# Performance work log

Hardware: AMD Instinct MI355X
Metric: run time of the kernel (lower is better)

The kernel has to match this reference:

```python
import jax, jax.numpy as jnp
import numpy as np

D_MODEL = 1024
H = 16
D_K = D_MODEL // H
B, S = 1, 4096


def setup_inputs() -> dict:
    key = jax.random.key(0)
    ks = jax.random.split(key, 12)
    std = 1.0 / np.sqrt(D_MODEL)
    inp = {
        "q": jax.random.normal(ks[0], (B, S, D_MODEL), dtype=jnp.float32),
        "k": jax.random.normal(ks[1], (B, S, D_MODEL), dtype=jnp.float32),
        "v": jax.random.normal(ks[2], (B, S, D_MODEL), dtype=jnp.float32),
        "mask": jax.random.randint(ks[3], (B, 1, S, S), 0, 2).astype(bool),
        # nn.Linear params (torch convention: y = x @ W.T + b), weights [out, in]
        "wq": jax.random.uniform(ks[4], (D_MODEL, D_MODEL), jnp.float32, -std, std),
        "bq": jax.random.uniform(ks[5], (D_MODEL,), jnp.float32, -std, std),
        "wk": jax.random.uniform(ks[6], (D_MODEL, D_MODEL), jnp.float32, -std, std),
        "bk": jax.random.uniform(ks[7], (D_MODEL,), jnp.float32, -std, std),
        "wv": jax.random.uniform(ks[8], (D_MODEL, D_MODEL), jnp.float32, -std, std),
        "bv": jax.random.uniform(ks[9], (D_MODEL,), jnp.float32, -std, std),
        "wo": jax.random.uniform(ks[10], (D_MODEL, D_MODEL), jnp.float32, -std, std),
        "bo": jax.random.uniform(ks[11], (D_MODEL,), jnp.float32, -std, std),
    }
    return inp


def _split_heads(x):
    # [b, s, (h d)] -> [b, h, s, d]
    b, s, _ = x.shape
    return x.reshape(b, s, H, D_K).transpose(0, 2, 1, 3)


def reference(q, k, v, mask, wq, bq, wk, bk, wv, bv, wo, bo):
    b, s, d = q.shape
    qh = _split_heads(q @ wq.T + bq)
    kh = _split_heads(k @ wk.T + bk)
    vh = _split_heads(v @ wv.T + bv)
    # NOTE: original scales by sqrt(d_model), not sqrt(d_k) — keep faithful.
    score = jnp.einsum("bhqd,bhkd->bhqk", qh, kh) / jnp.sqrt(jnp.float32(d))
    score = jnp.where(mask, jnp.float32(-1e9), score)
    attn = jax.nn.softmax(score, axis=-1)  # dropout is identity in eval mode
    wv_out = jnp.einsum("bhqk,bhkd->bhqd", attn, vh)
    concat = wv_out.transpose(0, 2, 1, 3).reshape(b, s, d)
    return concat @ wo.T + bo
```

## Files before the change

kernel.cpp:

```cpp
#include <hip/hip_runtime.h>
#include <hip/hip_bf16.h>
#include <math.h>

typedef __attribute__((ext_vector_type(4))) float f32x4;
typedef __attribute__((ext_vector_type(8))) short s16x8;
typedef __attribute__((ext_vector_type(4))) short s16x4;

#define S_LEN 4096
#define DMODEL 1024
#define NHEADS 16
#define DHEAD 64

__device__ __forceinline__ unsigned short f2bf(float f) {
  union { float f; unsigned int u; } x; x.f = f;
  return (unsigned short)((x.u + 0x7FFFu + ((x.u >> 16) & 1u)) >> 16);
}

__device__ __forceinline__ float fexp2(float x) {
#if __has_builtin(__builtin_amdgcn_exp2f)
  return __builtin_amdgcn_exp2f(x);
#else
  float r; asm("v_exp_f32 %0, %1" : "=v"(r) : "v"(x)); return r;
#endif
}

__device__ __forceinline__ void gload_lds16(const void* g, void* l) {
  __builtin_amdgcn_global_load_lds(
      (const __attribute__((address_space(1))) unsigned int*)g,
      (__attribute__((address_space(3))) unsigned int*)l, 16, 0, 0);
}

__global__ __launch_bounds__(256) void mask_pack(const int* __restrict__ mask,
                                                 unsigned long long* __restrict__ bits) {
  const int qr = blockIdx.x;
  const int wv = threadIdx.x >> 6, l = threadIdx.x & 63;
  const int* row = mask + (size_t)qr * S_LEN;
#pragma unroll
  for (int w0 = 0; w0 < 64; w0 += 4) {
    const int w = w0 + wv;
    unsigned long long b = __ballot(row[w * 64 + l] != 0);
    if (l == 0) bits[(size_t)qr * 64 + w] = b;
  }
}

__global__ __launch_bounds__(256) void mask_xpose(const unsigned long long* __restrict__ bits,
                                                  unsigned long long* __restrict__ lmask) {
  const int wv = blockIdx.x * 4 + (threadIdx.x >> 6);
  const int l = threadIdx.x & 63, lr = l & 15, lg4 = (l >> 4) * 4;
  const int qg = wv >> 6, t = wv & 63;
  const unsigned long long rw = bits[(size_t)(qg * 16 + lr) * 64 + t];
  unsigned long long mine = 0;
#pragma unroll
  for (int w = 0; w < 16; ++w) {
    const int sh = (w >> 2) * 16 + (w & 3) + lg4;
    unsigned long long b = __ballot(((rw >> sh) & 1ull) != 0);
    if (l == w) mine = b;
  }
  if (l < 16) lmask[((size_t)qg * 64 + t) * 16 + l] = mine;
}

__global__ __launch_bounds__(256) void cast_bf16(
    const float* __restrict__ s0, const float* __restrict__ s1, const float* __restrict__ s2,
    const float* __restrict__ s3, const float* __restrict__ s4, const float* __restrict__ s5,
    const float* __restrict__ s6, unsigned short* __restrict__ dst) {
  const int z = blockIdx.y;
  const float* src = (z == 0) ? s0 : (z == 1) ? s1 : (z == 2) ? s2 :
                     (z == 3) ? s3 : (z == 4) ? s4 : (z == 5) ? s5 : s6;
  const int n = (z < 3) ? (S_LEN * DMODEL) : (DMODEL * DMODEL);
  unsigned short* d = dst + ((z < 3) ? (size_t)z * S_LEN * DMODEL
                                     : (size_t)3 * S_LEN * DMODEL + (size_t)(z - 3) * DMODEL * DMODEL);
  const int i = (blockIdx.x * 256 + threadIdx.x) * 4;
  if (i < n) {
    f32x4 v = *(const f32x4*)(src + i);
    s16x4 o;
#pragma unroll
    for (int j = 0; j < 4; ++j) o[j] = (short)f2bf(v[j]);
    *(s16x4*)(d + i) = o;
  }
}

template<int A_BF16, int B_BF16, int OUT_MODE>
__device__ __forceinline__ void gemm_body(const void* __restrict__ Ap,
                                          const void* __restrict__ Wp,
                                          const float* __restrict__ bias,
                                          void* __restrict__ outp, float scale) {
  constexpr int K = DMODEL, N = DMODEL, M = S_LEN;
  constexpr int BM = 128, BK = 32, LDT = 40;
  __shared__ unsigned short Alds[BM * LDT];
  __shared__ unsigned short Blds[BM * LDT];
  const int tid = threadIdx.x;
  const int l = tid & 63, wid = tid >> 6;
  const int lr = l & 15, lg = l >> 4;
  const int bm = blockIdx.x * BM;
  const int bn = blockIdx.y * BM;
  const int wm = (wid >> 1) * 64, wn = (wid & 1) * 64;

  f32x4 acc[4][4] = {};

  for (int k0 = 0; k0 < K; k0 += BK) {
    __syncthreads();
    if constexpr (A_BF16) {
      const unsigned short* A = (const unsigned short*)Ap;
      const int col = (tid & 3) * 8, row = tid >> 2;
#pragma unroll
      for (int p = 0; p < 2; ++p) {
        const int r = row + p * 64;
        *(s16x8*)&Alds[r * LDT + col] =
            *(const s16x8*)(A + (size_t)(bm + r) * K + k0 + col);
      }
    } else {
      const float* A = (const float*)Ap;
      const int col = (tid & 7) * 4, row = tid >> 3;
#pragma unroll
      for (int p = 0; p < 4; ++p) {
        const int r = row + p * 32;
        f32x4 vv = *(const f32x4*)(A + (size_t)(bm + r) * K + k0 + col);
        s16x4 o;
#pragma unroll
        for (int j = 0; j < 4; ++j) o[j] = (short)f2bf(vv[j]);
        *(s16x4*)&Alds[r * LDT + col] = o;
      }
    }
    if constexpr (B_BF16) {
      const unsigned short* W = (const unsigned short*)Wp;
      const int col = (tid & 3) * 8, row = tid >> 2;
#pragma unroll
      for (int p = 0; p < 2; ++p) {
        const int r = row + p * 64;
        *(s16x8*)&Blds[r * LDT + col] =
            *(const s16x8*)(W + (size_t)(bn + r) * K + k0 + col);
      }
    } else {
      const float* W = (const float*)Wp;
      const int col = (tid & 7) * 4, row = tid >> 3;
#pragma unroll
      for (int p = 0; p < 4; ++p) {
        const int r = row + p * 32;
        f32x4 vv = *(const f32x4*)(W + (size_t)(bn + r) * K + k0 + col);
        s16x4 o;
#pragma unroll
        for (int j = 0; j < 4; ++j) o[j] = (short)f2bf(vv[j]);
        *(s16x4*)&Blds[r * LDT + col] = o;
      }
    }
    __syncthreads();
    s16x8 af[4], bfr[4];
#pragma unroll
    for (int mi = 0; mi < 4; ++mi)
      af[mi] = *(const s16x8*)&Alds[(wm + mi * 16 + lr) * LDT + lg * 8];
#pragma unroll
    for (int ni = 0; ni < 4; ++ni)
      bfr[ni] = *(const s16x8*)&Blds[(wn + ni * 16 + lr) * LDT + lg * 8];
#pragma unroll
    for (int mi = 0; mi < 4; ++mi)
#pragma unroll
      for (int ni = 0; ni < 4; ++ni)
        acc[mi][ni] = __builtin_amdgcn_mfma_f32_16x16x32_bf16(af[mi], bfr[ni], acc[mi][ni], 0, 0, 0);
  }

#pragma unroll
  for (int ni = 0; ni < 4; ++ni) {
    const int n = bn + wn + ni * 16 + lr;
    const float bv = bias[n];
#pragma unroll
    for (int mi = 0; mi < 4; ++mi) {
#pragma unroll
      for (int j = 0; j < 4; ++j) {
        const int m = bm + wm + mi * 16 + lg * 4 + j;
        const float val = (acc[mi][ni][j] + bv) * scale;
        if constexpr (OUT_MODE == 1) {
          unsigned short* out = (unsigned short*)outp;
          out[((size_t)(n >> 6) * M + m) * DHEAD + (n & 63)] = f2bf(val);
        } else if constexpr (OUT_MODE == 2) {
          unsigned short* out = (unsigned short*)outp;
          out[((size_t)(n >> 6) * DHEAD + (n & 63)) * M + m] = f2bf(val);
        } else {
          float* out = (float*)outp;
          out[(size_t)m * N + n] = val;
        }
      }
    }
  }
}

#define QSCALE 0.04508422f

__global__ __launch_bounds__(256) void proj_qkv_b16(
    const unsigned short* __restrict__ qb, const unsigned short* __restrict__ kb,
    const unsigned short* __restrict__ vb,
    const unsigned short* __restrict__ wqb, const float* __restrict__ bq,
    const unsigned short* __restrict__ wkb, const float* __restrict__ bk,
    const unsigned short* __restrict__ wvb, const float* __restrict__ bv,
    unsigned short* __restrict__ ws) {
  const int z = blockIdx.z;
  if (z == 0)      gemm_body<1, 1, 1>(qb, wqb, bq, ws, QSCALE);
  else if (z == 1) gemm_body<1, 1, 1>(kb, wkb, bk, ws + (size_t)S_LEN * DMODEL, 1.0f);
  else             gemm_body<1, 1, 2>(vb, wvb, bv, ws + (size_t)2 * S_LEN * DMODEL, 1.0f);
}
__global__ __launch_bounds__(256) void proj_qkv_f32(
    const float* __restrict__ q, const float* __restrict__ k, const float* __restrict__ v,
    const float* __restrict__ wq, const float* __restrict__ bq,
    const float* __restrict__ wk, const float* __restrict__ bk,
    const float* __restrict__ wv, const float* __restrict__ bv,
    unsigned short* __restrict__ ws) {
  const int z = blockIdx.z;
  if (z == 0)      gemm_body<0, 0, 1>(q, wq, bq, ws, QSCALE);
  else if (z == 1) gemm_body<0, 0, 1>(k, wk, bk, ws + (size_t)S_LEN * DMODEL, 1.0f);
  else             gemm_body<0, 0, 2>(v, wv, bv, ws + (size_t)2 * S_LEN * DMODEL, 1.0f);
}
__global__ __launch_bounds__(256) void outproj_b16(
    const unsigned short* __restrict__ concat, const unsigned short* __restrict__ wob,
    const float* __restrict__ bo, float* __restrict__ out) {
  gemm_body<1, 1, 0>(concat, wob, bo, out, 1.0f);
}
__global__ __launch_bounds__(256) void outproj_f32(
    const unsigned short* __restrict__ concat, const float* __restrict__ wo,
    const float* __restrict__ bo, float* __restrict__ out) {
  gemm_body<1, 0, 0>(concat, wo, bo, out, 1.0f);
}

template<int NSPLIT>
__global__ __launch_bounds__(512, 4) void attn_fwd(
    const unsigned short* __restrict__ Qh, const unsigned short* __restrict__ Kh,
    const unsigned short* __restrict__ Vt, const unsigned long long* __restrict__ lmask,
    unsigned short* __restrict__ outp,
    float* __restrict__ lpart) {
  __shared__ unsigned short Klds[2][64 * 64];
  __shared__ unsigned short Vlds[2][64 * 64];
  __shared__ unsigned short P_lds[8][32][72];

  const int tid = threadIdx.x;
  const int l = tid & 63, wid = tid >> 6;
  const int lr = l & 15, lg = l >> 4;
  const int per = 32 * NSPLIT;
  const int swz = (blockIdx.x & 7) * per + (blockIdx.x >> 3);
  const int h = swz / (16 * NSPLIT);
  const int split = (NSPLIT == 2) ? ((swz >> 4) & 1) : 0;
  const int qb = swz & 15;
  const int qrow0 = qb * 256 + wid * 32;
  const int kv0 = split * (S_LEN / NSPLIT);
  constexpr int NT = (S_LEN / NSPLIT) / 64;
  const int T0 = kv0 >> 6;

  const unsigned short* Qbase = Qh + ((size_t)h * S_LEN + qrow0) * DHEAD;
  s16x8 qf[2][2];
#pragma unroll
  for (int sub = 0; sub < 2; ++sub)
#pragma unroll
    for (int ds = 0; ds < 2; ++ds)
      qf[sub][ds] = *(const s16x8*)(Qbase + (sub * 16 + lr) * DHEAD + ds * 32 + lg * 8);

  const int wid_u = __builtin_amdgcn_readfirstlane(wid);
  const int qg0 = qb * 16 + wid_u * 2;
  const unsigned long long* mq0 = lmask + (size_t)qg0 * 64 * 16;
  const unsigned long long* mq1 = mq0 + (size_t)64 * 16;

  const int srow = l >> 3;
  const int schunk = (l & 7) ^ srow;
  const unsigned short* Kst = Kh + (size_t)h * S_LEN * DHEAD
                              + (size_t)(kv0 + wid * 8 + srow) * DHEAD + schunk * 8;
  const unsigned short* Vst = Vt + (size_t)h * DHEAD * S_LEN
                              + (size_t)(wid * 8 + srow) * S_LEN + kv0 + schunk * 8;
  const int sdst = (wid * 8) * 64;

  f32x4 o_acc[2][4] = {};
  float lsum[2] = {0.f, 0.f};

  gload_lds16(Kst, &Klds[0][sdst]);
  gload_lds16(Vst, &Vlds[0][sdst]);
  __syncthreads();

  const int xr = lr & 7;

  for (int t = 0; t < NT; ++t) {
    const int buf = t & 1;
    if (t < NT - 1) {
      gload_lds16(Kst + (size_t)(t + 1) * 64 * DHEAD, &Klds[buf ^ 1][sdst]);
      gload_lds16(Vst + (t + 1) * 64, &Vlds[buf ^ 1][sdst]);
    }

    const unsigned short* Kb = &Klds[buf][0];
    f32x4 sc[2][4];
    __builtin_amdgcn_s_setprio(1);
#pragma unroll
    for (int kg = 0; kg < 4; ++kg) {
      const int r = kg * 16 + lr;
      s16x8 k0 = *(const s16x8*)(Kb + r * 64 + ((lg ^ xr) * 8));
      s16x8 k1 = *(const s16x8*)(Kb + r * 64 + (((lg + 4) ^ xr) * 8));
#pragma unroll
      for (int sub = 0; sub < 2; ++sub) {
        f32x4 z = {};
        z = __builtin_amdgcn_mfma_f32_16x16x32_bf16(k0, qf[sub][0], z, 0, 0, 0);
        sc[sub][kg] = __builtin_amdgcn_mfma_f32_16x16x32_bf16(k1, qf[sub][1], z, 0, 0, 0);
      }
    }
    __builtin_amdgcn_s_setprio(0);

    const size_t mo = (size_t)(T0 + t) * 16;
#pragma unroll
    for (int sub = 0; sub < 2; ++sub) {
      const unsigned long long* qp = (sub ? mq1 : mq0) + mo;
#pragma unroll
      for (int kg = 0; kg < 4; ++kg) {
        float p[4];
#pragma unroll
        for (int j = 0; j < 4; ++j) {
          const unsigned long long mw = qp[kg * 4 + j];
          float pv = fexp2(sc[sub][kg][j]);
          asm("v_cndmask_b32 %0, %1, 0, %2" : "=v"(pv) : "v"(pv), "s"(mw));
          p[j] = pv;
          lsum[sub] += pv;
        }
        unsigned int w0, w1;
        asm("v_cvt_pk_bf16_f32 %0, %1, %2" : "=v"(w0) : "v"(p[0]), "v"(p[1]));
        asm("v_cvt_pk_bf16_f32 %0, %1, %2" : "=v"(w1) : "v"(p[2]), "v"(p[3]));
        uint2 pk; pk.x = w0; pk.y = w1;
        *(uint2*)&P_lds[wid][sub * 16 + lr][kg * 16 + lg * 4] = pk;
      }
    }
    asm volatile("s_waitcnt lgkmcnt(0)" ::: "memory");
    __builtin_amdgcn_sched_barrier(0);

    s16x8 pf[2][2];
#pragma unroll
    for (int sub = 0; sub < 2; ++sub)
#pragma unroll
      for (int ks = 0; ks < 2; ++ks)
        pf[sub][ks] = *(const s16x8*)&P_lds[wid][sub * 16 + lr][ks * 32 + lg * 8];

    const unsigned short* Vb = &Vlds[buf][0];
    __builtin_amdgcn_s_setprio(1);
#pragma unroll
    for (int dg = 0; dg < 4; ++dg) {
      const int r = dg * 16 + lr;
      s16x8 v0 = *(const s16x8*)(Vb + r * 64 + ((lg ^ xr) * 8));
      s16x8 v1 = *(const s16x8*)(Vb + r * 64 + (((lg + 4) ^ xr) * 8));
#pragma unroll
      for (int sub = 0; sub < 2; ++sub) {
        o_acc[sub][dg] = __builtin_amdgcn_mfma_f32_16x16x32_bf16(pf[sub][0], v0, o_acc[sub][dg], 0, 0, 0);
        o_acc[sub][dg] = __builtin_amdgcn_mfma_f32_16x16x32_bf16(pf[sub][1], v1, o_acc[sub][dg], 0, 0, 0);
      }
    }
    __builtin_amdgcn_s_setprio(0);

    __syncthreads();
  }

#pragma unroll
  for (int sub = 0; sub < 2; ++sub) {
    lsum[sub] += __shfl_xor(lsum[sub], 16, 64);
    lsum[sub] += __shfl_xor(lsum[sub], 32, 64);
  }

  if constexpr (NSPLIT == 2) {
    unsigned short* op = outp + ((size_t)(split * NHEADS + h) * S_LEN) * DHEAD;
#pragma unroll
    for (int sub = 0; sub < 2; ++sub)
#pragma unroll
      for (int dg = 0; dg < 4; ++dg)
#pragma unroll
        for (int j = 0; j < 4; ++j) {
          const int q = qrow0 + sub * 16 + lg * 4 + j;
          op[(size_t)q * DHEAD + dg * 16 + lr] = f2bf(o_acc[sub][dg][j]);
        }
    if (l < 16) {
      float* lp = lpart + (size_t)(split * NHEADS + h) * S_LEN + qrow0;
      lp[lr] = lsum[0];
      lp[16 + lr] = lsum[1];
    }
  } else {
    float rs[2][4];
#pragma unroll
    for (int sub = 0; sub < 2; ++sub)
#pragma unroll
      for (int j = 0; j < 4; ++j)
        rs[sub][j] = __shfl(lsum[sub], lg * 4 + j, 64);
#pragma unroll
    for (int sub = 0; sub < 2; ++sub)
#pragma unroll
      for (int dg = 0; dg < 4; ++dg)
#pragma unroll
        for (int j = 0; j < 4; ++j) {
          const int q = qrow0 + sub * 16 + lg * 4 + j;
          outp[(size_t)q * DMODEL + h * DHEAD + dg * 16 + lr] =
              f2bf(o_acc[sub][dg][j] / rs[sub][j]);
        }
  }
}

__global__ __launch_bounds__(256) void attn_combine(
    const unsigned short* __restrict__ opart, const float* __restrict__ lpart,
    unsigned short* __restrict__ concat) {
  const int idx = blockIdx.x * 256 + threadIdx.x;
  const int d4 = (idx & 15) * 4;
  const int hq = idx >> 4;
  const int h = hq >> 12, q = hq & 4095;
  const size_t o0 = ((size_t)h * S_LEN + q) * DHEAD + d4;
  const size_t o1 = o0 + (size_t)NHEADS * S_LEN * DHEAD;
  const float linv = 1.0f / (lpart[(size_t)h * S_LEN + q] +
                             lpart[(size_t)(NHEADS + h) * S_LEN + q]);
  s16x4 a = *(const s16x4*)(opart + o0);
  s16x4 b = *(const s16x4*)(opart + o1);
  s16x4 r;
#pragma unroll
  for (int i = 0; i < 4; ++i) {
    union { unsigned int u; float f; } xa, xb;
    xa.u = ((unsigned int)(unsigned short)a[i]) << 16;
    xb.u = ((unsigned int)(unsigned short)b[i]) << 16;
    r[i] = (short)f2bf((xa.f + xb.f) * linv);
  }
  *(s16x4*)(concat + ((size_t)q * DMODEL + h * DHEAD + d4)) = r;
}

extern "C" void kernel_launch(void* const* d_in, const int* in_sizes, int n_in,
                              void* d_out, int out_size, void* d_ws, size_t ws_size,
                              hipStream_t stream) {
  const float* q  = (const float*)d_in[0];
  const float* k  = (const float*)d_in[1];
  const float* v  = (const float*)d_in[2];
  const int* mask = (const int*)d_in[3];
  const float* wq = (const float*)d_in[4];
  const float* bq = (const float*)d_in[5];
  const float* wk = (const float*)d_in[6];
  const float* bk = (const float*)d_in[7];
  const float* wv = (const float*)d_in[8];
  const float* bv = (const float*)d_in[9];
  const float* wo = (const float*)d_in[10];
  const float* bo = (const float*)d_in[11];
  float* out = (float*)d_out;

  const size_t SD = (size_t)S_LEN * DMODEL, DD = (size_t)DMODEL * DMODEL;
  unsigned short* wsq = (unsigned short*)d_ws;
  unsigned short* wsc = wsq + 3 * SD;
  unsigned long long* wsbits = (unsigned long long*)(wsc + SD);
  unsigned long long* wslm = wsbits + (size_t)S_LEN * 64;
  unsigned short* cast0 = (unsigned short*)(wslm + (size_t)256 * 64 * 16);
  const size_t need = (size_t)((char*)(cast0 + 3 * SD + 4 * DD) - (char*)d_ws);
  const bool big = ws_size >= need;

  mask_pack<<<dim3(S_LEN), dim3(256), 0, stream>>>(mask, wsbits);
  mask_xpose<<<dim3(4096), dim3(256), 0, stream>>>(wsbits, wslm);

  if (big) {
    unsigned short* qb  = cast0;
    unsigned short* kb  = qb + SD;
    unsigned short* vb  = kb + SD;
    unsigned short* wqb = vb + SD;
    unsigned short* wkb = wqb + DD;
    unsigned short* wvb = wkb + DD;
    unsigned short* wob = wvb + DD;
    unsigned short* opart = cast0;
    float* lpart = (float*)vb;
    cast_bf16<<<dim3(4096, 7), dim3(256), 0, stream>>>(q, k, v, wq, wk, wv, wo, cast0);
    proj_qkv_b16<<<dim3(32, 8, 3), dim3(256), 0, stream>>>(qb, kb, vb, wqb, bq, wkb, bk, wvb, bv, wsq);
    attn_fwd<2><<<dim3(512), dim3(512), 0, stream>>>(wsq, wsq + SD, wsq + 2 * SD, wslm, opart, lpart);
    attn_combine<<<dim3(4096), dim3(256), 0, stream>>>(opart, lpart, wsc);
    outproj_b16<<<dim3(32, 8), dim3(256), 0, stream>>>(wsc, wob, bo, out);
  } else {
    proj_qkv_f32<<<dim3(32, 8, 3), dim3(256), 0, stream>>>(q, k, v, wq, bq, wk, bk, wv, bv, wsq);
    attn_fwd<1><<<dim3(256), dim3(512), 0, stream>>>(wsq, wsq + SD, wsq + 2 * SD, wslm, wsc, nullptr);
    outproj_f32<<<dim3(32, 8), dim3(256), 0, stream>>>(wsc, wo, bo, out);
  }
}
```

Before: 199.1 us.

## Fuse mask packing into one kernel and use direct-to-LDS loads in bf16 GEMM

Measured after the change: 219.1 us. 10.1% more time.

```diff
diff --git a/kernel.cpp b/kernel.cpp
--- a/kernel.cpp
+++ b/kernel.cpp
@@ -30,33 +30,22 @@
       (__attribute__((address_space(3))) unsigned int*)l, 16, 0, 0);
 }
 
-__global__ __launch_bounds__(256) void mask_pack(const int* __restrict__ mask,
-                                                 unsigned long long* __restrict__ bits) {
-  const int qr = blockIdx.x;
+__global__ __launch_bounds__(256) void mask_lane(const int* __restrict__ mask,
+                                                 unsigned long long* __restrict__ lmask) {
+  const int qg = blockIdx.x;
   const int wv = threadIdx.x >> 6, l = threadIdx.x & 63;
-  const int* row = mask + (size_t)qr * S_LEN;
-#pragma unroll
-  for (int w0 = 0; w0 < 64; w0 += 4) {
-    const int w = w0 + wv;
-    unsigned long long b = __ballot(row[w * 64 + l] != 0);
-    if (l == 0) bits[(size_t)qr * 64 + w] = b;
-  }
-}
-
-__global__ __launch_bounds__(256) void mask_xpose(const unsigned long long* __restrict__ bits,
-                                                  unsigned long long* __restrict__ lmask) {
-  const int wv = blockIdx.x * 4 + (threadIdx.x >> 6);
-  const int l = threadIdx.x & 63, lr = l & 15, lg4 = (l >> 4) * 4;
-  const int qg = wv >> 6, t = wv & 63;
-  const unsigned long long rw = bits[(size_t)(qg * 16 + lr) * 64 + t];
-  unsigned long long mine = 0;
-#pragma unroll
-  for (int w = 0; w < 16; ++w) {
-    const int sh = (w >> 2) * 16 + (w & 3) + lg4;
-    unsigned long long b = __ballot(((rw >> sh) & 1ull) != 0);
-    if (l == w) mine = b;
-  }
-  if (l < 16) lmask[((size_t)qg * 64 + t) * 16 + l] = mine;
+  const int lr = l & 15, lg = l >> 4;
+  const int* base = mask + (size_t)(qg * 16 + lr) * S_LEN;
+  for (int t = wv; t < 64; t += 4) {
+#pragma unroll
+    for (int kg = 0; kg < 4; ++kg) {
+#pragma unroll
+      for (int j = 0; j < 4; ++j) {
+        unsigned long long b = __ballot(base[t * 64 + kg * 16 + lg * 4 + j] != 0);
+        if (l == 0) lmask[((size_t)qg * 64 + t) * 16 + kg * 4 + j] = b;
+      }
+    }
+  }
 }
 
 __global__ __launch_bounds__(256) void cast_bf16(
@@ -79,78 +68,46 @@
   }
 }
 
-template<int A_BF16, int B_BF16, int OUT_MODE>
-__device__ __forceinline__ void gemm_body(const void* __restrict__ Ap,
-                                          const void* __restrict__ Wp,
-                                          const float* __restrict__ bias,
-                                          void* __restrict__ outp, float scale) {
+template<int OUT_MODE>
+__device__ __forceinline__ void gemm_b16_body(const unsigned short* __restrict__ A,
+                                              const unsigned short* __restrict__ W,
+                                              const float* __restrict__ bias,
+                                              void* __restrict__ outp, float scale) {
   constexpr int K = DMODEL, N = DMODEL, M = S_LEN;
-  constexpr int BM = 128, BK = 32, LDT = 40;
-  __shared__ unsigned short Alds[BM * LDT];
-  __shared__ unsigned short Blds[BM * LDT];
+  constexpr int BM = 128, BK = 32;
+  __shared__ unsigned short Alds[BM * BK];
+  __shared__ unsigned short Blds[BM * BK];
   const int tid = threadIdx.x;
   const int l = tid & 63, wid = tid >> 6;
   const int lr = l & 15, lg = l >> 4;
-  const int bm = blockIdx.x * BM;
-  const int bn = blockIdx.y * BM;
+  const int bm = blockIdx.x * BM, bn = blockIdx.y * BM;
   const int wm = (wid >> 1) * 64, wn = (wid & 1) * 64;
 
+  const int srow = tid >> 2;
+  const int schunk = (tid & 3) ^ (srow & 3);
+  const unsigned short* As = A + (size_t)(bm + srow) * K + schunk * 8;
+  const unsigned short* Ws = W + (size_t)(bn + srow) * K + schunk * 8;
+  unsigned short* Ald = &Alds[srow * BK + (tid & 3) * 8];
+  unsigned short* Bld = &Blds[srow * BK + (tid & 3) * 8];
+
   f32x4 acc[4][4] = {};
+  const int xc = (lg ^ (lr & 3)) * 8;
 
   for (int k0 = 0; k0 < K; k0 += BK) {
     __syncthreads();
-    if constexpr (A_BF16) {
-      const unsigned short* A = (const unsigned short*)Ap;
-      const int col = (tid & 3) * 8, row = tid >> 2;
-#pragma unroll
-      for (int p = 0; p < 2; ++p) {
-        const int r = row + p * 64;
-        *(s16x8*)&Alds[r * LDT + col] =
-            *(const s16x8*)(A + (size_t)(bm + r) * K + k0 + col);
-      }
-    } else {
-      const float* A = (const float*)Ap;
-      const int col = (tid & 7) * 4, row = tid >> 3;
-#pragma unroll
-      for (int p = 0; p < 4; ++p) {
-        const int r = row + p * 32;
-        f32x4 vv = *(const f32x4*)(A + (size_t)(bm + r) * K + k0 + col);
-        s16x4 o;
-#pragma unroll
-        for (int j = 0; j < 4; ++j) o[j] = (short)f2bf(vv[j]);
-        *(s16x4*)&Alds[r * LDT + col] = o;
-      }
-    }
-    if constexpr (B_BF16) {
-      const unsigned short* W = (const unsigned short*)Wp;
-      const int col = (tid & 3) * 8, row = tid >> 2;
-#pragma unroll
-      for (int p = 0; p < 2; ++p) {
-        const int r = row + p * 64;
-        *(s16x8*)&Blds[r * LDT + col] =
-            *(const s16x8*)(W + (size_t)(bn + r) * K + k0 + col);
-      }
-    } else {
-      const float* W = (const float*)Wp;
-      const int col = (tid & 7) * 4, row = tid >> 3;
-#pragma unroll
-      for (int p = 0; p < 4; ++p) {
-        const int r = row + p * 32;
-        f32x4 vv = *(const f32x4*)(W + (size_t)(bn + r) * K + k0 + col);
-        s16x4 o;
-#pragma unroll
-        for (int j = 0; j < 4; ++j) o[j] = (short)f2bf(vv[j]);
-        *(s16x4*)&Blds[r * LDT + col] = o;
-      }
-    }
+    gload_lds16(As + k0, Ald);
+    gload_lds16(As + (size_t)64 * K + k0, Ald + 64 * BK);
+    gload_lds16(Ws + k0, Bld);
+    gload_lds16(Ws + (size_t)64 * K + k0, Bld + 64 * BK);
     __syncthreads();
+
     s16x8 af[4], bfr[4];
 #pragma unroll
     for (int mi = 0; mi < 4; ++mi)
-      af[mi] = *(const s16x8*)&Alds[(wm + mi * 16 + lr) * LDT + lg * 8];
+      af[mi] = *(const s16x8*)&Alds[(wm + mi * 16 + lr) * BK + xc];
 #pragma unroll
     for (int ni = 0; ni < 4; ++ni)
-      bfr[ni] = *(const s16x8*)&Blds[(wn + ni * 16 + lr) * LDT + lg * 8];
+      bfr[ni] = *(const s16x8*)&Blds[(wn + ni * 16 + lr) * BK + xc];
 #pragma unroll
     for (int mi = 0; mi < 4; ++mi)
 #pragma unroll
@@ -183,6 +140,101 @@
   }
 }
 
+template<int A_BF16, int OUT_MODE>
+__device__ __forceinline__ void gemm_f32_body(const void* __restrict__ Ap,
+                                              const float* __restrict__ W,
+                                              const float* __restrict__ bias,
+                                              void* __restrict__ outp, float scale) {
+  constexpr int K = DMODEL, N = DMODEL, M = S_LEN;
+  constexpr int BM = 128, BK = 32, LDT = 40;
+  __shared__ unsigned short Alds[BM * LDT];
+  __shared__ unsigned short Blds[BM * LDT];
+  const int tid = threadIdx.x;
+  const int l = tid & 63, wid = tid >> 6;
+  const int lr = l & 15, lg = l >> 4;
+  const int bm = blockIdx.x * BM;
+  const int bn = blockIdx.y * BM;
+  const int wm = (wid >> 1) * 64, wn = (wid & 1) * 64;
+
+  f32x4 acc[4][4] = {};
+
+  for (int k0 = 0; k0 < K; k0 += BK) {
+    __syncthreads();
+    if constexpr (A_BF16) {
+      const unsigned short* A = (const unsigned short*)Ap;
+      const int col = (tid & 3) * 8, row = tid >> 2;
+#pragma unroll
+      for (int p = 0; p < 2; ++p) {
+        const int r = row + p * 64;
+        *(s16x8*)&Alds[r * LDT + col] =
+            *(const s16x8*)(A + (size_t)(bm + r) * K + k0 + col);
+      }
+    } else {
+      const float* A = (const float*)Ap;
+      const int col = (tid & 7) * 4, row = tid >> 3;
+#pragma unroll
+      for (int p = 0; p < 4; ++p) {
+        const int r = row + p * 32;
+        f32x4 vv = *(const f32x4*)(A + (size_t)(bm + r) * K + k0 + col);
+        s16x4 o;
+#pragma unroll
+        for (int j = 0; j < 4; ++j) o[j] = (short)f2bf(vv[j]);
+        *(s16x4*)&Alds[r * LDT + col] = o;
+      }
+    }
+    {
+      const float* Wf = W;
+      const int col = (tid & 7) * 4, row = tid >> 3;
+#pragma unroll
+      for (int p = 0; p < 4; ++p) {
+        const int r = row + p * 32;
+        f32x4 vv = *(const f32x4*)(Wf + (size_t)(bn + r) * K + k0 + col);
+        s16x4 o;
+#pragma unroll
+        for (int j = 0; j < 4; ++j) o[j] = (short)f2bf(vv[j]);
+        *(s16x4*)&Blds[r * LDT + col] = o;
+      }
+    }
+    __syncthreads();
+    s16x8 af[4], bfr[4];
+#pragma unroll
+    for (int mi = 0; mi < 4; ++mi)
+      af[mi] = *(const s16x8*)&Alds[(wm + mi * 16 + lr) * LDT + lg * 8];
+#pragma unroll
+    for (int ni = 0; ni < 4; ++ni)
+      bfr[ni] = *(const s16x8*)&Blds[(wn + ni * 16 + lr) * LDT + lg * 8];
+#pragma unroll
+    for (int mi = 0; mi < 4; ++mi)
+#pragma unroll
+      for (int ni = 0; ni < 4; ++ni)
+        acc[mi][ni] = __builtin_amdgcn_mfma_f32_16x16x32_bf16(af[mi], bfr[ni], acc[mi][ni], 0, 0, 0);
+  }
+
+#pragma unroll
+  for (int ni = 0; ni < 4; ++ni) {
+    const int n = bn + wn + ni * 16 + lr;
+    const float bv = bias[n];
+#pragma unroll
+    for (int mi = 0; mi < 4; ++mi) {
+#pragma unroll
+      for (int j = 0; j < 4; ++j) {
+        const int m = bm + wm + mi * 16 + lg * 4 + j;
+        const float val = (acc[mi][ni][j] + bv) * scale;
+        if constexpr (OUT_MODE == 1) {
+          unsigned short* out = (unsigned short*)outp;
+          out[((size_t)(n >> 6) * M + m) * DHEAD + (n & 63)] = f2bf(val);
+        } else if constexpr (OUT_MODE == 2) {
+          unsigned short* out = (unsigned short*)outp;
+          out[((size_t)(n >> 6) * DHEAD + (n & 63)) * M + m] = f2bf(val);
+        } else {
+          float* out = (float*)outp;
+          out[(size_t)m * N + n] = val;
+        }
+      }
+    }
+  }
+}
+
 #define QSCALE 0.04508422f
 
 __global__ __launch_bounds__(256) void proj_qkv_b16(
@@ -193,9 +245,14 @@
     const unsigned short* __restrict__ wvb, const float* __restrict__ bv,
     unsigned short* __restrict__ ws) {
   const int z = blockIdx.z;
-  if (z == 0)      gemm_body<1, 1, 1>(qb, wqb, bq, ws, QSCALE);
-  else if (z == 1) gemm_body<1, 1, 1>(kb, wkb, bk, ws + (size_t)S_LEN * DMODEL, 1.0f);
-  else             gemm_body<1, 1, 2>(vb, wvb, bv, ws + (size_t)2 * S_LEN * DMODEL, 1.0f);
+  if (z == 0)      gemm_b16_body<1>(qb, wqb, bq, ws, QSCALE);
+  else if (z == 1) gemm_b16_body<1>(kb, wkb, bk, ws + (size_t)S_LEN * DMODEL, 1.0f);
+  else             gemm_b16_body<2>(vb, wvb, bv, ws + (size_t)2 * S_LEN * DMODEL, 1.0f);
+}
+__global__ __launch_bounds__(256) void outproj_b16(
+    const unsigned short* __restrict__ concat, const unsigned short* __restrict__ wob,
+    const float* __restrict__ bo, float* __restrict__ out) {
+  gemm_b16_body<0>(concat, wob, bo, out, 1.0f);
 }
 __global__ __launch_bounds__(256) void proj_qkv_f32(
     const float* __restrict__ q, const float* __restrict__ k, const float* __restrict__ v,
@@ -204,19 +261,14 @@
     const float* __restrict__ wv, const float* __restrict__ bv,
     unsigned short* __restrict__ ws) {
   const int z = blockIdx.z;
-  if (z == 0)      gemm_body<0, 0, 1>(q, wq, bq, ws, QSCALE);
-  else if (z == 1) gemm_body<0, 0, 1>(k, wk, bk, ws + (size_t)S_LEN * DMODEL, 1.0f);
-  else             gemm_body<0, 0, 2>(v, wv, bv, ws + (size_t)2 * S_LEN * DMODEL, 1.0f);
-}
-__global__ __launch_bounds__(256) void outproj_b16(
-    const unsigned short* __restrict__ concat, const unsigned short* __restrict__ wob,
-    const float* __restrict__ bo, float* __restrict__ out) {
-  gemm_body<1, 1, 0>(concat, wob, bo, out, 1.0f);
+  if (z == 0)      gemm_f32_body<0, 1>(q, wq, bq, ws, QSCALE);
+  else if (z == 1) gemm_f32_body<0, 1>(k, wk, bk, ws + (size_t)S_LEN * DMODEL, 1.0f);
+  else             gemm_f32_body<0, 2>(v, wv, bv, ws + (size_t)2 * S_LEN * DMODEL, 1.0f);
 }
 __global__ __launch_bounds__(256) void outproj_f32(
     const unsigned short* __restrict__ concat, const float* __restrict__ wo,
     const float* __restrict__ bo, float* __restrict__ out) {
-  gemm_body<1, 0, 0>(concat, wo, bo, out, 1.0f);
+  gemm_f32_body<1, 0>(concat, wo, bo, out, 1.0f);
 }
 
 template<int NSPLIT>
@@ -227,7 +279,7 @@
     float* __restrict__ lpart) {
   __shared__ unsigned short Klds[2][64 * 64];
   __shared__ unsigned short Vlds[2][64 * 64];
-  __shared__ unsigned short P_lds[8][32][72];
+  __shared__ unsigned short P_lds[8][32][76];
 
   const int tid = threadIdx.x;
   const int l = tid & 63, wid = tid >> 6;
@@ -432,14 +484,12 @@
   const size_t SD = (size_t)S_LEN * DMODEL, DD = (size_t)DMODEL * DMODEL;
   unsigned short* wsq = (unsigned short*)d_ws;
   unsigned short* wsc = wsq + 3 * SD;
-  unsigned long long* wsbits = (unsigned long long*)(wsc + SD);
-  unsigned long long* wslm = wsbits + (size_t)S_LEN * 64;
+  unsigned long long* wslm = (unsigned long long*)(wsc + SD);
   unsigned short* cast0 = (unsigned short*)(wslm + (size_t)256 * 64 * 16);
   const size_t need = (size_t)((char*)(cast0 + 3 * SD + 4 * DD) - (char*)d_ws);
   const bool big = ws_size >= need;
 
-  mask_pack<<<dim3(S_LEN), dim3(256), 0, stream>>>(mask, wsbits);
-  mask_xpose<<<dim3(4096), dim3(256), 0, stream>>>(wsbits, wslm);
+  mask_lane<<<dim3(256), dim3(256), 0, stream>>>(mask, wslm);
 
   if (big) {
     unsigned short* qb  = cast0;
```

## Fuse mask packing into single pass and merge with bf16 cast kernel

Applied to the files above, without the earlier changes.

New measurement: 208.8 us. 4.9% more time.

```diff
diff --git a/kernel.cpp b/kernel.cpp
--- a/kernel.cpp
+++ b/kernel.cpp
@@ -30,40 +30,37 @@
       (__attribute__((address_space(3))) unsigned int*)l, 16, 0, 0);
 }
 
-__global__ __launch_bounds__(256) void mask_pack(const int* __restrict__ mask,
-                                                 unsigned long long* __restrict__ bits) {
-  const int qr = blockIdx.x;
-  const int wv = threadIdx.x >> 6, l = threadIdx.x & 63;
-  const int* row = mask + (size_t)qr * S_LEN;
-#pragma unroll
-  for (int w0 = 0; w0 < 64; w0 += 4) {
-    const int w = w0 + wv;
-    unsigned long long b = __ballot(row[w * 64 + l] != 0);
-    if (l == 0) bits[(size_t)qr * 64 + w] = b;
-  }
-}
-
-__global__ __launch_bounds__(256) void mask_xpose(const unsigned long long* __restrict__ bits,
-                                                  unsigned long long* __restrict__ lmask) {
-  const int wv = blockIdx.x * 4 + (threadIdx.x >> 6);
-  const int l = threadIdx.x & 63, lr = l & 15, lg4 = (l >> 4) * 4;
-  const int qg = wv >> 6, t = wv & 63;
-  const unsigned long long rw = bits[(size_t)(qg * 16 + lr) * 64 + t];
-  unsigned long long mine = 0;
-#pragma unroll
-  for (int w = 0; w < 16; ++w) {
-    const int sh = (w >> 2) * 16 + (w & 3) + lg4;
-    unsigned long long b = __ballot(((rw >> sh) & 1ull) != 0);
-    if (l == w) mine = b;
-  }
-  if (l < 16) lmask[((size_t)qg * 64 + t) * 16 + l] = mine;
-}
-
-__global__ __launch_bounds__(256) void cast_bf16(
+__device__ __forceinline__ void mask_lane_body(const int* __restrict__ mask,
+                                               unsigned long long* __restrict__ lmask,
+                                               int qg, int tchunk) {
+  const int t = tchunk * 4 + (threadIdx.x >> 6);
+  const int l = threadIdx.x & 63, lr = l & 15, lg = l >> 4;
+  const int* base = mask + (size_t)(qg * 16 + lr) * S_LEN + t * 64;
+#pragma unroll
+  for (int kg = 0; kg < 4; ++kg) {
+#pragma unroll
+    for (int j = 0; j < 4; ++j) {
+      unsigned long long b = __ballot(base[kg * 16 + lg * 4 + j] != 0);
+      if (l == 0) lmask[((size_t)qg * 64 + t) * 16 + kg * 4 + j] = b;
+    }
+  }
+}
+
+__global__ __launch_bounds__(256) void mask_lane(const int* __restrict__ mask,
+                                                 unsigned long long* __restrict__ lmask) {
+  mask_lane_body(mask, lmask, blockIdx.x, blockIdx.y);
+}
+
+__global__ __launch_bounds__(256) void prep_fused(
     const float* __restrict__ s0, const float* __restrict__ s1, const float* __restrict__ s2,
     const float* __restrict__ s3, const float* __restrict__ s4, const float* __restrict__ s5,
-    const float* __restrict__ s6, unsigned short* __restrict__ dst) {
+    const float* __restrict__ s6, unsigned short* __restrict__ dst,
+    const int* __restrict__ mask, unsigned long long* __restrict__ lmask) {
   const int z = blockIdx.y;
+  if (z == 7) {
+    mask_lane_body(mask, lmask, blockIdx.x >> 4, blockIdx.x & 15);
+    return;
+  }
   const float* src = (z == 0) ? s0 : (z == 1) ? s1 : (z == 2) ? s2 :
                      (z == 3) ? s3 : (z == 4) ? s4 : (z == 5) ? s5 : s6;
   const int n = (z < 3) ? (S_LEN * DMODEL) : (DMODEL * DMODEL);
@@ -197,6 +194,11 @@
   else if (z == 1) gemm_body<1, 1, 1>(kb, wkb, bk, ws + (size_t)S_LEN * DMODEL, 1.0f);
   else             gemm_body<1, 1, 2>(vb, wvb, bv, ws + (size_t)2 * S_LEN * DMODEL, 1.0f);
 }
+__global__ __launch_bounds__(256) void outproj_b16(
+    const unsigned short* __restrict__ concat, const unsigned short* __restrict__ wob,
+    const float* __restrict__ bo, float* __restrict__ out) {
+  gemm_body<1, 1, 0>(concat, wob, bo, out, 1.0f);
+}
 __global__ __launch_bounds__(256) void proj_qkv_f32(
     const float* __restrict__ q, const float* __restrict__ k, const float* __restrict__ v,
     const float* __restrict__ wq, const float* __restrict__ bq,
@@ -208,11 +210,6 @@
   else if (z == 1) gemm_body<0, 0, 1>(k, wk, bk, ws + (size_t)S_LEN * DMODEL, 1.0f);
   else             gemm_body<0, 0, 2>(v, wv, bv, ws + (size_t)2 * S_LEN * DMODEL, 1.0f);
 }
-__global__ __launch_bounds__(256) void outproj_b16(
-    const unsigned short* __restrict__ concat, const unsigned short* __restrict__ wob,
-    const float* __restrict__ bo, float* __restrict__ out) {
-  gemm_body<1, 1, 0>(concat, wob, bo, out, 1.0f);
-}
 __global__ __launch_bounds__(256) void outproj_f32(
     const unsigned short* __restrict__ concat, const float* __restrict__ wo,
     const float* __restrict__ bo, float* __restrict__ out) {
@@ -227,7 +224,7 @@
     float* __restrict__ lpart) {
   __shared__ unsigned short Klds[2][64 * 64];
   __shared__ unsigned short Vlds[2][64 * 64];
-  __shared__ unsigned short P_lds[8][32][72];
+  __shared__ unsigned short P_lds[8][32][76];
 
   const int tid = threadIdx.x;
   const int l = tid & 63, wid = tid >> 6;
@@ -432,14 +429,10 @@
   const size_t SD = (size_t)S_LEN * DMODEL, DD = (size_t)DMODEL * DMODEL;
   unsigned short* wsq = (unsigned short*)d_ws;
   unsigned short* wsc = wsq + 3 * SD;
-  unsigned long long* wsbits = (unsigned long long*)(wsc + SD);
-  unsigned long long* wslm = wsbits + (size_t)S_LEN * 64;
+  unsigned long long* wslm = (unsigned long long*)(wsc + SD);
   unsigned short* cast0 = (unsigned short*)(wslm + (size_t)256 * 64 * 16);
   const size_t need = (size_t)((char*)(cast0 + 3 * SD + 4 * DD) - (char*)d_ws);
   const bool big = ws_size >= need;
-
-  mask_pack<<<dim3(S_LEN), dim3(256), 0, stream>>>(mask, wsbits);
-  mask_xpose<<<dim3(4096), dim3(256), 0, stream>>>(wsbits, wslm);
 
   if (big) {
     unsigned short* qb  = cast0;
@@ -451,12 +444,14 @@
     unsigned short* wob = wvb + DD;
     unsigned short* opart = cast0;
     float* lpart = (float*)vb;
-    cast_bf16<<<dim3(4096, 7), dim3(256), 0, stream>>>(q, k, v, wq, wk, wv, wo, cast0);
+    prep_fused<<<dim3(4096, 8), dim3(256), 0, stream>>>(q, k, v, wq, wk, wv, wo,
+                                                        cast0, mask, wslm);
     proj_qkv_b16<<<dim3(32, 8, 3), dim3(256), 0, stream>>>(qb, kb, vb, wqb, bq, wkb, bk, wvb, bv, wsq);
     attn_fwd<2><<<dim3(512), dim3(512), 0, stream>>>(wsq, wsq + SD, wsq + 2 * SD, wslm, opart, lpart);
     attn_combine<<<dim3(4096), dim3(256), 0, stream>>>(opart, lpart, wsc);
     outproj_b16<<<dim3(32, 8), dim3(256), 0, stream>>>(wsc, wob, bo, out);
   } else {
+    mask_lane<<<dim3(256, 16), dim3(256), 0, stream>>>(mask, wslm);
     proj_qkv_f32<<<dim3(32, 8, 3), dim3(256), 0, stream>>>(q, k, v, wq, bq, wk, bk, wv, bv, wsq);
     attn_fwd<1><<<dim3(256), dim3(512), 0, stream>>>(wsq, wsq + SD, wsq + 2 * SD, wslm, wsc, nullptr);
     outproj_f32<<<dim3(32, 8), dim3(256), 0, stream>>>(wsc, wo, bo, out);
```
